# Kernel tuning notes

Hardware: AMD Instinct MI355X
Metric: run time of the kernel (lower is better)

The kernel has to match this reference:

```python
import jax, jax.numpy as jnp
import numpy as np

K = 1024          # num_embeddings
D = 128           # embedding_dim
COMMITMENT_COST = 0.25


def setup_inputs() -> dict:
    key = jax.random.key(0)
    k1, k2 = jax.random.split(key)
    inputs = jax.random.normal(k1, (16, D, 4096), dtype=jnp.float32)
    codebook = jax.random.normal(k2, (K, D), dtype=jnp.float32)
    return {"inputs": inputs, "codebook": codebook}


def reference(inputs, codebook):
    # inputs: [B, D, T]; codebook: [K, D]
    B, Dd, T = inputs.shape
    flat = jnp.transpose(inputs, (0, 2, 1)).reshape(-1, Dd)  # [N, D], N = B*T
    N = flat.shape[0]

    d = (jnp.sum(flat * flat, axis=1, keepdims=True)
         + jnp.sum(codebook * codebook, axis=1)
         - 2.0 * flat @ codebook.T)
    idx = jnp.argmin(d, axis=1)  # [N]

    # gather-based quantization (same math as one-hot @ codebook)
    quantized = codebook[idx]                                   # [N, D]
    quantized = quantized.reshape(B, T, Dd).transpose(0, 2, 1)  # [B, D, T]

    # commitment loss (quantized detached; stop_gradient irrelevant in fwd)
    e_latent_loss = jnp.mean((jax.lax.stop_gradient(quantized) - inputs) ** 2)
    loss = COMMITMENT_COST * e_latent_loss

    # straight-through estimator
    quantized_st = inputs + jax.lax.stop_gradient(quantized - inputs)

    # perplexity from code usage histogram (= mean of one-hot encodings)
    counts = jnp.zeros((codebook.shape[0],), dtype=jnp.float32).at[idx].add(1.0)
    avg_probs = counts / N
    perplexity = jnp.exp(-jnp.sum(avg_probs * jnp.log(avg_probs + 1e-10)))

    return loss, quantized_st, perplexity, idx.reshape(B, T)
```

## Files before the change

kernel.cpp:

```cpp
#include <hip/hip_runtime.h>

#define T_FULL 4096
#define D 128
#define K 1024
#define NVEC 65536
#define BDT 8388608
#define BT 128
#define NBLK (NVEC / BT)
#define KT 32
#define NIT (K / KT)
#define PLANE_B (K * D * 2)
#define TILE_B (3 * KT * D * 2)

typedef unsigned short ushort_t;
typedef __bf16 bf16x8 __attribute__((ext_vector_type(8)));
typedef float f32x4 __attribute__((ext_vector_type(4)));

__device__ __forceinline__ float trunc_bf(float x, ushort_t* bits) {
  union { float f; unsigned u; } a; a.f = x;
  *bits = (ushort_t)(a.u >> 16);
  union { unsigned u; float f; } b; b.u = a.u & 0xFFFF0000u;
  return b.f;
}
__device__ __forceinline__ __bf16 bf_bits(ushort_t u) {
  union { ushort_t u; __bf16 h; } c; c.u = u; return c.h;
}

#define MFMA(a, b, c) __builtin_amdgcn_mfma_f32_16x16x32_bf16((a), (b), (c), 0, 0, 0)

#define GLOAD_LDS(g, l)                                                        \
  __builtin_amdgcn_global_load_lds(                                            \
      (const __attribute__((address_space(1))) unsigned int*)(g),              \
      (__attribute__((address_space(3))) unsigned int*)(l), 16, 0, 0)

__global__ __launch_bounds__(128) void prep_kernel(const float* __restrict__ cb,
    float* __restrict__ ee, ushort_t* __restrict__ Eh, ushort_t* __restrict__ Em,
    ushort_t* __restrict__ El, unsigned int* __restrict__ counts,
    unsigned int* __restrict__ done, float* __restrict__ loss_acc) {
  int k = blockIdx.x, d = threadIdx.x;
  if (d == 0) {
    counts[k] = 0u;
    if (k == 0) { *done = 0u; *loss_acc = 0.f; }
  }
  float e = cb[k * D + d];
  float v = e * e;
#pragma unroll
  for (int o = 32; o > 0; o >>= 1) v += __shfl_down(v, o, 64);
  __shared__ float tmp[2];
  if ((d & 63) == 0) tmp[d >> 6] = v;
  __syncthreads();
  if (d == 0) ee[k] = tmp[0] + tmp[1];

  float s = 2.0f * e;
  ushort_t hb, mb, lb;
  float hf = trunc_bf(s, &hb);
  float r  = s - hf;
  float mf = trunc_bf(r, &mb);
  (void)trunc_bf(r - mf, &lb);
  Eh[k * D + d] = hb; Em[k * D + d] = mb; El[k * D + d] = lb;
}

__global__ __launch_bounds__(256, 2) void vq_main(
    const float* __restrict__ inp, const float* __restrict__ cb,
    const float* __restrict__ ee, const ushort_t* __restrict__ Eplanes,
    unsigned int* __restrict__ counts, unsigned int* __restrict__ done,
    float* __restrict__ loss_acc, float* __restrict__ out) {
  __shared__ __align__(16) ushort_t Bs[2 * 3 * KT * D];
  __shared__ float ee_sh[K];
  __shared__ int   midx[BT];
  __shared__ float lred[4];
  __shared__ int   lastf;

  float* out_q   = out + 1;
  float* out_idx = out + 2 + BDT;

  const int tid  = threadIdx.x;
  const int lane = tid & 63;
  const int w    = tid >> 6;
  const int c    = lane & 15;
  const int q    = lane >> 4;
  const int b    = blockIdx.x >> 5;
  const int t0   = (blockIdx.x & 31) * BT;

  unsigned soff[6], sldsoff[6];
#pragma unroll
  for (int i = 0; i < 6; ++i) {
    int flatb = w * 384 + i * 64;
    int p     = flatb >> 9;
    int s     = (flatb & 511) + lane;
    int code  = s >> 4;
    int dg    = (s & 15) ^ (code & 15);
    soff[i]    = (unsigned)(p * PLANE_B + code * 256 + dg * 16);
    sldsoff[i] = (unsigned)(flatb * 16);
  }
  const char* Eb = (const char*)Eplanes;

#pragma unroll
  for (int i = 0; i < 6; ++i)
    GLOAD_LDS(Eb + soff[i], (char*)Bs + sldsoff[i]);

  bf16x8 Ah[2][4], Am[2][4], Al[2][4];
  {
    const float* xin = inp + (size_t)b * D * T_FULL + t0 + w * 32 + c;
#pragma unroll
    for (int n = 0; n < 2; ++n)
#pragma unroll
      for (int dci = 0; dci < 4; ++dci) {
        const int dcg = (dci + w) & 3;
        bf16x8 ah, am, al;
#pragma unroll
        for (int j = 0; j < 8; ++j) {
          int d = dcg * 32 + q * 8 + j;
          float x = xin[(size_t)d * T_FULL + n * 16];
          ushort_t hb, mb, lb;
          float hf = trunc_bf(x, &hb);
          float r  = x - hf;
          float mf = trunc_bf(r, &mb);
          (void)trunc_bf(r - mf, &lb);
          ah[j] = bf_bits(hb); am[j] = bf_bits(mb); al[j] = bf_bits(lb);
        }
        Ah[n][dci] = ah; Am[n][dci] = am; Al[n][dci] = al;
      }
  }
#pragma unroll
  for (int i = tid; i < K; i += 256) ee_sh[i] = ee[i];
  __syncthreads();

  float bv[2][4];
  int   bi[2][4];
#pragma unroll
  for (int n = 0; n < 2; ++n)
#pragma unroll
    for (int r = 0; r < 4; ++r) { bv[n][r] = 3.4e38f; bi[n][r] = 0; }

  for (int it = 0; it < NIT; ++it) {
    const int kt = it * KT;
    const int bb = it & 1;

    {
      const int ktn = (kt + KT) & (K - 1);
      const unsigned lb = (unsigned)((bb ^ 1) * TILE_B);
#pragma unroll
      for (int i = 0; i < 6; ++i)
        GLOAD_LDS(Eb + (size_t)ktn * 256 + soff[i], (char*)Bs + lb + sldsoff[i]);
    }

    f32x4 acc[2][2];
#pragma unroll
    for (int n = 0; n < 2; ++n)
#pragma unroll
      for (int kf = 0; kf < 2; ++kf) acc[n][kf] = (f32x4){0.f, 0.f, 0.f, 0.f};

    const char* Bp = (const char*)Bs + bb * TILE_B;
#pragma unroll
    for (int dci = 0; dci < 4; ++dci) {
      const int dcg = (dci + w) & 3;
      const int sw = ((dcg * 4 + q) ^ c) * 16;
      bf16x8 Bh[2], Bm[2], Bl[2];
#pragma unroll
      for (int kf = 0; kf < 2; ++kf) {
        const int ro = (kf * 16 + c) * 256 + sw;
        Bh[kf] = *(const bf16x8*)(Bp + ro);
        Bm[kf] = *(const bf16x8*)(Bp + 8192 + ro);
        Bl[kf] = *(const bf16x8*)(Bp + 16384 + ro);
      }
#pragma unroll
      for (int n = 0; n < 2; ++n)
#pragma unroll
        for (int kf = 0; kf < 2; ++kf) {
          f32x4 a = acc[n][kf];
          a = MFMA(Ah[n][dci], Bh[kf], a);
          a = MFMA(Ah[n][dci], Bm[kf], a);
          a = MFMA(Am[n][dci], Bh[kf], a);
          a = MFMA(Ah[n][dci], Bl[kf], a);
          a = MFMA(Al[n][dci], Bh[kf], a);
          a = MFMA(Am[n][dci], Bm[kf], a);
          acc[n][kf] = a;
        }
    }

#pragma unroll
    for (int kf = 0; kf < 2; ++kf) {
      const int code = kt + kf * 16 + c;
      const float eev = ee_sh[code];
#pragma unroll
      for (int n = 0; n < 2; ++n)
#pragma unroll
        for (int r = 0; r < 4; ++r) {
          float dist = eev - acc[n][kf][r];
          if (dist < bv[n][r]) { bv[n][r] = dist; bi[n][r] = code; }
        }
    }
    __syncthreads();
  }

#pragma unroll
  for (int m = 1; m <= 8; m <<= 1)
#pragma unroll
    for (int n = 0; n < 2; ++n)
#pragma unroll
      for (int r = 0; r < 4; ++r) {
        float ov = __shfl_xor(bv[n][r], m, 64);
        int   oi = __shfl_xor(bi[n][r], m, 64);
        if (ov < bv[n][r] || (ov == bv[n][r] && oi < bi[n][r])) {
          bv[n][r] = ov; bi[n][r] = oi;
        }
      }
  if (c == 0) {
#pragma unroll
    for (int n = 0; n < 2; ++n)
#pragma unroll
      for (int r = 0; r < 4; ++r)
        midx[w * 32 + n * 16 + q * 4 + r] = bi[n][r];
  }
  __syncthreads();

  if (tid < BT) {
    int ki = midx[tid];
    out_idx[(size_t)b * T_FULL + t0 + tid] = (float)ki;
    atomicAdd(&counts[ki], 1u);
  }

  float lsum = 0.f;
#pragma unroll
  for (int n = 0; n < 2; ++n) {
    const int tn = w * 32 + n * 16 + c;
    const int kq = midx[tn];
    const float* crow = cb + (size_t)kq * D;
    float* qbase = out_q + (size_t)b * D * T_FULL + t0 + tn;
#pragma unroll
    for (int dci = 0; dci < 4; ++dci) {
      const int dcg = (dci + w) & 3;
      const int d0 = dcg * 32 + q * 8;
      float4 qa = *(const float4*)(crow + d0);
      float4 qb = *(const float4*)(crow + d0 + 4);
      float qv[8] = {qa.x, qa.y, qa.z, qa.w, qb.x, qb.y, qb.z, qb.w};
#pragma unroll
      for (int j = 0; j < 8; ++j) {
        float x = (float)Ah[n][dci][j] + (float)Am[n][dci][j] + (float)Al[n][dci][j];
        float df = qv[j] - x;
        lsum = fmaf(df, df, lsum);
        qbase[(size_t)(d0 + j) * T_FULL] = qv[j];
      }
    }
  }
#pragma unroll
  for (int o = 32; o > 0; o >>= 1) lsum += __shfl_down(lsum, o, 64);
  if (lane == 0) lred[w] = lsum;
  __syncthreads();
  if (tid == 0) {
    atomicAdd(loss_acc, lred[0] + lred[1] + lred[2] + lred[3]);
    __threadfence();
    unsigned ticket = atomicAdd(done, 1u);
    lastf = (ticket == NBLK - 1) ? 1 : 0;
  }
  __syncthreads();

  if (lastf) {
    __threadfence();
    float ent = 0.f;
#pragma unroll
    for (int i = tid; i < K; i += 256) {
      float cnt = (float)atomicAdd(&counts[i], 0u);
      float p = cnt * (1.0f / (float)NVEC);
      ent = fmaf(p, logf(p + 1e-10f), ent);
    }
#pragma unroll
    for (int o = 32; o > 0; o >>= 1) ent += __shfl_down(ent, o, 64);
    if (lane == 0) lred[w] = ent;
    __syncthreads();
    if (tid == 0) {
      float e = lred[0] + lred[1] + lred[2] + lred[3];
      float l = atomicAdd(loss_acc, 0.f);
      out[0]       = 0.25f * (l / (float)BDT);
      out[1 + BDT] = expf(-e);
    }
  }
}

extern "C" void kernel_launch(void* const* d_in, const int* in_sizes, int n_in,
                              void* d_out, int out_size, void* d_ws, size_t ws_size,
                              hipStream_t stream) {
  const float* inp = (const float*)d_in[0];
  const float* cb  = (const float*)d_in[1];
  float* out = (float*)d_out;

  char* ws = (char*)d_ws;
  unsigned int* counts  = (unsigned int*)ws;
  unsigned int* done    = (unsigned int*)(ws + 4096);
  float*        lossacc = (float*)(ws + 4160);
  float*        ee      = (float*)(ws + 8192);
  ushort_t*     Eh      = (ushort_t*)(ws + 12288);
  ushort_t*     Em      = (ushort_t*)(ws + 12288 + PLANE_B);
  ushort_t*     El      = (ushort_t*)(ws + 12288 + 2 * PLANE_B);

  prep_kernel<<<K, 128, 0, stream>>>(cb, ee, Eh, Em, El, counts, done, lossacc);
  vq_main<<<NBLK, 256, 0, stream>>>(inp, cb, ee, Eh, counts, done, lossacc, out);
}
```

Measured before the change: 215.0 us.

## Switch distance GEMM from three-way bf16 split to two-way fp16 split

Replaces the bf16 hi/mid/lo decomposition of inputs and codebook (6 MFMAs per tile pair) with an fp16 hi/lo split that needs only 4 MFMAs and two codebook planes. This cuts matrix-core work, LDS tile size and codebook staging traffic. The block is also halved to 128 threads covering 64 vectors, with the per-wave k-chunk rotation removed, so the launch now has more, smaller blocks. The two-term fp16 split carries slightly less precision than the three-term bf16 split and relies on fp16 range, which could flip near-tie argmin results.

```diff
diff --git a/kernel.cpp b/kernel.cpp
--- a/kernel.cpp
+++ b/kernel.cpp
@@ -5,28 +5,17 @@
 #define K 1024
 #define NVEC 65536
 #define BDT 8388608
-#define BT 128
+#define BT 64
 #define NBLK (NVEC / BT)
 #define KT 32
 #define NIT (K / KT)
 #define PLANE_B (K * D * 2)
-#define TILE_B (3 * KT * D * 2)
-
-typedef unsigned short ushort_t;
-typedef __bf16 bf16x8 __attribute__((ext_vector_type(8)));
+#define TILE_B (2 * KT * D * 2)
+
+typedef _Float16 f16x8 __attribute__((ext_vector_type(8)));
 typedef float f32x4 __attribute__((ext_vector_type(4)));
 
-__device__ __forceinline__ float trunc_bf(float x, ushort_t* bits) {
-  union { float f; unsigned u; } a; a.f = x;
-  *bits = (ushort_t)(a.u >> 16);
-  union { unsigned u; float f; } b; b.u = a.u & 0xFFFF0000u;
-  return b.f;
-}
-__device__ __forceinline__ __bf16 bf_bits(ushort_t u) {
-  union { ushort_t u; __bf16 h; } c; c.u = u; return c.h;
-}
-
-#define MFMA(a, b, c) __builtin_amdgcn_mfma_f32_16x16x32_bf16((a), (b), (c), 0, 0, 0)
+#define MFMA(a, b, c) __builtin_amdgcn_mfma_f32_16x16x32_f16((a), (b), (c), 0, 0, 0)
 
 #define GLOAD_LDS(g, l)                                                        \
   __builtin_amdgcn_global_load_lds(                                            \
@@ -34,9 +23,9 @@
       (__attribute__((address_space(3))) unsigned int*)(l), 16, 0, 0)
 
 __global__ __launch_bounds__(128) void prep_kernel(const float* __restrict__ cb,
-    float* __restrict__ ee, ushort_t* __restrict__ Eh, ushort_t* __restrict__ Em,
-    ushort_t* __restrict__ El, unsigned int* __restrict__ counts,
-    unsigned int* __restrict__ done, float* __restrict__ loss_acc) {
+    float* __restrict__ ee, _Float16* __restrict__ E1, _Float16* __restrict__ E2,
+    unsigned int* __restrict__ counts, unsigned int* __restrict__ done,
+    float* __restrict__ loss_acc) {
   int k = blockIdx.x, d = threadIdx.x;
   if (d == 0) {
     counts[k] = 0u;
@@ -52,23 +41,21 @@
   if (d == 0) ee[k] = tmp[0] + tmp[1];
 
   float s = 2.0f * e;
-  ushort_t hb, mb, lb;
-  float hf = trunc_bf(s, &hb);
-  float r  = s - hf;
-  float mf = trunc_bf(r, &mb);
-  (void)trunc_bf(r - mf, &lb);
-  Eh[k * D + d] = hb; Em[k * D + d] = mb; El[k * D + d] = lb;
+  _Float16 h1 = (_Float16)s;
+  _Float16 h2 = (_Float16)(s - (float)h1);
+  E1[k * D + d] = h1;
+  E2[k * D + d] = h2;
 }
 
-__global__ __launch_bounds__(256, 2) void vq_main(
+__global__ __launch_bounds__(128, 2) void vq_main(
     const float* __restrict__ inp, const float* __restrict__ cb,
-    const float* __restrict__ ee, const ushort_t* __restrict__ Eplanes,
+    const float* __restrict__ ee, const _Float16* __restrict__ Eplanes,
     unsigned int* __restrict__ counts, unsigned int* __restrict__ done,
     float* __restrict__ loss_acc, float* __restrict__ out) {
-  __shared__ __align__(16) ushort_t Bs[2 * 3 * KT * D];
+  __shared__ __align__(16) _Float16 Bs[2 * 2 * KT * D];
   __shared__ float ee_sh[K];
   __shared__ int   midx[BT];
-  __shared__ float lred[4];
+  __shared__ float lred[2];
   __shared__ int   lastf;
 
   float* out_q   = out + 1;
@@ -79,51 +66,48 @@
   const int w    = tid >> 6;
   const int c    = lane & 15;
   const int q    = lane >> 4;
-  const int b    = blockIdx.x >> 5;
-  const int t0   = (blockIdx.x & 31) * BT;
-
-  unsigned soff[6], sldsoff[6];
-#pragma unroll
-  for (int i = 0; i < 6; ++i) {
-    int flatb = w * 384 + i * 64;
-    int p     = flatb >> 9;
-    int s     = (flatb & 511) + lane;
-    int code  = s >> 4;
-    int dg    = (s & 15) ^ (code & 15);
-    soff[i]    = (unsigned)(p * PLANE_B + code * 256 + dg * 16);
-    sldsoff[i] = (unsigned)(flatb * 16);
+  const int b    = blockIdx.x >> 6;
+  const int t0   = (blockIdx.x & 63) * BT;
+
+  unsigned soff[8], slds[8];
+#pragma unroll
+  for (int i = 0; i < 8; ++i) {
+    int flat = tid + i * 128;
+    int p    = flat >> 9;
+    int s    = flat & 511;
+    int code = s >> 4;
+    int dgp  = s & 15;
+    int dg   = dgp ^ (code & 15);
+    soff[i] = (unsigned)(p * PLANE_B + code * 256 + dg * 16);
+    slds[i] = (unsigned)(flat * 16);
   }
   const char* Eb = (const char*)Eplanes;
 
 #pragma unroll
-  for (int i = 0; i < 6; ++i)
-    GLOAD_LDS(Eb + soff[i], (char*)Bs + sldsoff[i]);
-
-  bf16x8 Ah[2][4], Am[2][4], Al[2][4];
+  for (int i = 0; i < 8; ++i)
+    GLOAD_LDS(Eb + soff[i], (char*)Bs + slds[i]);
+
+  f16x8 A1[2][4], A2[2][4];
   {
     const float* xin = inp + (size_t)b * D * T_FULL + t0 + w * 32 + c;
 #pragma unroll
     for (int n = 0; n < 2; ++n)
 #pragma unroll
-      for (int dci = 0; dci < 4; ++dci) {
-        const int dcg = (dci + w) & 3;
-        bf16x8 ah, am, al;
+      for (int dc = 0; dc < 4; ++dc) {
+        f16x8 a1, a2;
 #pragma unroll
         for (int j = 0; j < 8; ++j) {
-          int d = dcg * 32 + q * 8 + j;
+          int d = dc * 32 + q * 8 + j;
           float x = xin[(size_t)d * T_FULL + n * 16];
-          ushort_t hb, mb, lb;
-          float hf = trunc_bf(x, &hb);
-          float r  = x - hf;
-          float mf = trunc_bf(r, &mb);
-          (void)trunc_bf(r - mf, &lb);
-          ah[j] = bf_bits(hb); am[j] = bf_bits(mb); al[j] = bf_bits(lb);
-        }
-        Ah[n][dci] = ah; Am[n][dci] = am; Al[n][dci] = al;
-      }
-  }
-#pragma unroll
-  for (int i = tid; i < K; i += 256) ee_sh[i] = ee[i];
+          _Float16 h1 = (_Float16)x;
+          _Float16 h2 = (_Float16)(x - (float)h1);
+          a1[j] = h1; a2[j] = h2;
+        }
+        A1[n][dc] = a1; A2[n][dc] = a2;
+      }
+  }
+#pragma unroll
+  for (int i = tid; i < K; i += 128) ee_sh[i] = ee[i];
   __syncthreads();
 
   float bv[2][4];
@@ -139,10 +123,10 @@
 
     {
       const int ktn = (kt + KT) & (K - 1);
-      const unsigned lb = (unsigned)((bb ^ 1) * TILE_B);
-#pragma unroll
-      for (int i = 0; i < 6; ++i)
-        GLOAD_LDS(Eb + (size_t)ktn * 256 + soff[i], (char*)Bs + lb + sldsoff[i]);
+      const unsigned lbo = (unsigned)((bb ^ 1) * TILE_B);
+#pragma unroll
+      for (int i = 0; i < 8; ++i)
+        GLOAD_LDS(Eb + (size_t)ktn * 256 + soff[i], (char*)Bs + lbo + slds[i]);
     }
 
     f32x4 acc[2][2];
@@ -153,28 +137,24 @@
 
     const char* Bp = (const char*)Bs + bb * TILE_B;
 #pragma unroll
-    for (int dci = 0; dci < 4; ++dci) {
-      const int dcg = (dci + w) & 3;
-      const int sw = ((dcg * 4 + q) ^ c) * 16;
-      bf16x8 Bh[2], Bm[2], Bl[2];
+    for (int dc = 0; dc < 4; ++dc) {
+      const int sw = ((dc * 4 + q) ^ c) * 16;
+      f16x8 B1[2], B2[2];
 #pragma unroll
       for (int kf = 0; kf < 2; ++kf) {
         const int ro = (kf * 16 + c) * 256 + sw;
-        Bh[kf] = *(const bf16x8*)(Bp + ro);
-        Bm[kf] = *(const bf16x8*)(Bp + 8192 + ro);
-        Bl[kf] = *(const bf16x8*)(Bp + 16384 + ro);
+        B1[kf] = *(const f16x8*)(Bp + ro);
+        B2[kf] = *(const f16x8*)(Bp + 8192 + ro);
       }
 #pragma unroll
       for (int n = 0; n < 2; ++n)
 #pragma unroll
         for (int kf = 0; kf < 2; ++kf) {
           f32x4 a = acc[n][kf];
-          a = MFMA(Ah[n][dci], Bh[kf], a);
-          a = MFMA(Ah[n][dci], Bm[kf], a);
-          a = MFMA(Am[n][dci], Bh[kf], a);
-          a = MFMA(Ah[n][dci], Bl[kf], a);
-          a = MFMA(Al[n][dci], Bh[kf], a);
-          a = MFMA(Am[n][dci], Bm[kf], a);
+          a = MFMA(A1[n][dc], B1[kf], a);
+          a = MFMA(A1[n][dc], B2[kf], a);
+          a = MFMA(A2[n][dc], B1[kf], a);
+          a = MFMA(A2[n][dc], B2[kf], a);
           acc[n][kf] = a;
         }
     }
@@ -229,15 +209,14 @@
     const float* crow = cb + (size_t)kq * D;
     float* qbase = out_q + (size_t)b * D * T_FULL + t0 + tn;
 #pragma unroll
-    for (int dci = 0; dci < 4; ++dci) {
-      const int dcg = (dci + w) & 3;
-      const int d0 = dcg * 32 + q * 8;
+    for (int dc = 0; dc < 4; ++dc) {
+      const int d0 = dc * 32 + q * 8;
       float4 qa = *(const float4*)(crow + d0);
       float4 qb = *(const float4*)(crow + d0 + 4);
       float qv[8] = {qa.x, qa.y, qa.z, qa.w, qb.x, qb.y, qb.z, qb.w};
 #pragma unroll
       for (int j = 0; j < 8; ++j) {
-        float x = (float)Ah[n][dci][j] + (float)Am[n][dci][j] + (float)Al[n][dci][j];
+        float x = (float)A1[n][dc][j] + (float)A2[n][dc][j];
         float df = qv[j] - x;
         lsum = fmaf(df, df, lsum);
         qbase[(size_t)(d0 + j) * T_FULL] = qv[j];
@@ -249,7 +228,7 @@
   if (lane == 0) lred[w] = lsum;
   __syncthreads();
   if (tid == 0) {
-    atomicAdd(loss_acc, lred[0] + lred[1] + lred[2] + lred[3]);
+    atomicAdd(loss_acc, lred[0] + lred[1]);
     __threadfence();
     unsigned ticket = atomicAdd(done, 1u);
     lastf = (ticket == NBLK - 1) ? 1 : 0;
@@ -260,7 +239,7 @@
     __threadfence();
     float ent = 0.f;
 #pragma unroll
-    for (int i = tid; i < K; i += 256) {
+    for (int i = tid; i < K; i += 128) {
       float cnt = (float)atomicAdd(&counts[i], 0u);
       float p = cnt * (1.0f / (float)NVEC);
       ent = fmaf(p, logf(p + 1e-10f), ent);
@@ -270,7 +249,7 @@
     if (lane == 0) lred[w] = ent;
     __syncthreads();
     if (tid == 0) {
-      float e = lred[0] + lred[1] + lred[2] + lred[3];
+      float e = lred[0] + lred[1];
       float l = atomicAdd(loss_acc, 0.f);
       out[0]       = 0.25f * (l / (float)BDT);
       out[1 + BDT] = expf(-e);
@@ -290,10 +269,9 @@
   unsigned int* done    = (unsigned int*)(ws + 4096);
   float*        lossacc = (float*)(ws + 4160);
   float*        ee      = (float*)(ws + 8192);
-  ushort_t*     Eh      = (ushort_t*)(ws + 12288);
-  ushort_t*     Em      = (ushort_t*)(ws + 12288 + PLANE_B);
-  ushort_t*     El      = (ushort_t*)(ws + 12288 + 2 * PLANE_B);
-
-  prep_kernel<<<K, 128, 0, stream>>>(cb, ee, Eh, Em, El, counts, done, lossacc);
-  vq_main<<<NBLK, 256, 0, stream>>>(inp, cb, ee, Eh, counts, done, lossacc, out);
+  _Float16*     E1      = (_Float16*)(ws + 12288);
+  _Float16*     E2      = (_Float16*)(ws + 12288 + PLANE_B);
+
+  prep_kernel<<<K, 128, 0, stream>>>(cb, ee, E1, E2, counts, done, lossacc);
+  vq_main<<<NBLK, 128, 0, stream>>>(inp, cb, ee, E1, counts, done, lossacc, out);
 }
```

Result: slower. 223.8 us (+4.1%).
